# Optimization experiments

Measured on AMD Instinct MI355X. Metric: run time of the kernel, lower is better.

Reference implementation:

```python
import jax, jax.numpy as jnp
import numpy as np

NUM_EXPERTS = 8
TOP_K = 2
HIDDEN = 1024
INTER = 1408


def setup_inputs() -> dict:
    key = jax.random.key(0)
    k0, k1, k2, k3, k4 = jax.random.split(key, 5)
    B, S = 2, 2048
    d_scale = HIDDEN ** -0.5
    i_scale = INTER ** -0.5
    return {
        "hidden_states": jax.random.normal(k0, (B, S, HIDDEN), jnp.float32),
        # nn.Linear(hidden, num_experts, bias=False): weight (E, d)
        "gate_w": jax.random.normal(k1, (NUM_EXPERTS, HIDDEN), jnp.float32) * d_scale,
        # per-expert SwiGLU weights, nn.Linear convention (out, in)
        "gate_proj": jax.random.normal(k2, (NUM_EXPERTS, INTER, HIDDEN), jnp.float32) * d_scale,
        "up_proj": jax.random.normal(k3, (NUM_EXPERTS, INTER, HIDDEN), jnp.float32) * d_scale,
        "down_proj": jax.random.normal(k4, (NUM_EXPERTS, HIDDEN, INTER), jnp.float32) * i_scale,
    }


def reference(hidden_states, gate_w, gate_proj, up_proj, down_proj):
    B, S, D = hidden_states.shape
    x = hidden_states.reshape(-1, D)  # (T, d)
    T = x.shape[0]

    # gate linear -> router logits (T, E)
    router_logits = x @ gate_w.T

    # TopKRouter: softmax in fp32 over all experts, top-k, optional renorm
    probs = jax.nn.softmax(router_logits.astype(jnp.float32), axis=-1)
    routing_weights, selected_experts = jax.lax.top_k(probs, TOP_K)  # (T, k)
    routing_weights = routing_weights / routing_weights.sum(axis=-1, keepdims=True)  # norm_topk_prob
    routing_weights = routing_weights.astype(x.dtype)

    # combine weights per (token, expert): scatter top-k weights into dense (T, E)
    combine = jnp.zeros((T, NUM_EXPERTS), x.dtype).at[
        jnp.arange(T)[:, None], selected_experts
    ].add(routing_weights)

    # per-expert SwiGLU FFN, weighted combine (loop over small fixed expert set)
    out = jnp.zeros_like(x)
    for e in range(NUM_EXPERTS):
        h = jax.nn.silu(x @ gate_proj[e].T) * (x @ up_proj[e].T)  # (T, i)
        out = out + combine[:, e : e + 1] * (h @ down_proj[e].T)  # (T, d)

    return out.reshape(B, S, D), router_logits
```

## Files before the change

### kernel.cpp

```cpp
#include <hip/hip_runtime.h>
#include <hip/hip_bf16.h>
#include <stdint.h>

#define T_TOK 4096
#define DH 1024
#define DI 1408
#define NE 8
#define TOPK 2
#define PADROWS 9216

typedef short s16x8 __attribute__((ext_vector_type(8)));
typedef float f32x4 __attribute__((ext_vector_type(4)));

__device__ inline unsigned f2bf(float f) {
    __hip_bfloat16 h = __float2bfloat16(f);
    return (unsigned)*(unsigned short*)&h;
}
__device__ inline float bf2f(unsigned short u) {
    return __uint_as_float(((unsigned)u) << 16);
}

#define GLDS(src, dst) __builtin_amdgcn_global_load_lds( \
    (const __attribute__((address_space(1))) void*)(src), \
    (__attribute__((address_space(3))) void*)(dst), 16, 0, 0)

__global__ __launch_bounds__(256) void router_kernel(const float* __restrict__ x,
                              const float* __restrict__ gw,
                              float* __restrict__ logits_out,
                              int* __restrict__ tokE, float* __restrict__ tokW,
                              unsigned short* __restrict__ xb,
                              const float* __restrict__ gp, const float* __restrict__ up,
                              const float* __restrict__ dp,
                              unsigned short* __restrict__ gpb, unsigned short* __restrict__ upb,
                              unsigned short* __restrict__ dpb) {
    int wave = threadIdx.x >> 6;
    int lane = threadIdx.x & 63;
    int t = blockIdx.x * 4 + wave;
    const float4* xr = (const float4*)(x + (size_t)t * DH);

    float acc[NE];
#pragma unroll
    for (int e = 0; e < NE; ++e) acc[e] = 0.f;

#pragma unroll
    for (int i = 0; i < 4; ++i) {
        float4 xv = xr[lane + i * 64];
#pragma unroll
        for (int e = 0; e < NE; ++e) {
            float4 g = ((const float4*)(gw + (size_t)e * DH))[lane + i * 64];
            acc[e] += xv.x * g.x + xv.y * g.y + xv.z * g.z + xv.w * g.w;
        }
        uint2 o;
        o.x = f2bf(xv.x) | (f2bf(xv.y) << 16);
        o.y = f2bf(xv.z) | (f2bf(xv.w) << 16);
        *(uint2*)(xb + (size_t)t * DH + (lane + i * 64) * 4) = o;
    }
#pragma unroll
    for (int e = 0; e < NE; ++e) {
#pragma unroll
        for (int off = 32; off > 0; off >>= 1) acc[e] += __shfl_xor(acc[e], off, 64);
    }
    if (lane == 0) {
        float mx = acc[0];
#pragma unroll
        for (int e = 1; e < NE; ++e) mx = fmaxf(mx, acc[e]);
        float p[NE]; float s = 0.f;
#pragma unroll
        for (int e = 0; e < NE; ++e) { p[e] = expf(acc[e] - mx); s += p[e]; }
        float inv = 1.f / s;
#pragma unroll
        for (int e = 0; e < NE; ++e) p[e] *= inv;
        int i0 = 0, i1 = -1; float p0 = -1.f, p1 = -1.f;
#pragma unroll
        for (int e = 0; e < NE; ++e) {
            float v = p[e];
            if (v > p0) { p1 = p0; i1 = i0; p0 = v; i0 = e; }
            else if (v > p1) { p1 = v; i1 = e; }
        }
        float wsum = p0 + p1;
#pragma unroll
        for (int e = 0; e < NE; ++e) logits_out[(size_t)t * NE + e] = acc[e];
        tokE[2 * t]     = i0;  tokE[2 * t + 1] = i1;
        tokW[2 * t]     = p0 / wsum;  tokW[2 * t + 1] = p1 / wsum;
    }

    const int NW4 = NE * DI * DH / 4;
    const int NT = (T_TOK / 4) * 256;
    int gtid = blockIdx.x * 256 + threadIdx.x;
    for (int i = gtid; i < NW4; i += NT) {
        float4 v = ((const float4*)gp)[i];
        uint2 o;
        o.x = f2bf(v.x) | (f2bf(v.y) << 16);
        o.y = f2bf(v.z) | (f2bf(v.w) << 16);
        ((uint2*)gpb)[i] = o;
    }
    for (int i = gtid; i < NW4; i += NT) {
        float4 v = ((const float4*)up)[i];
        uint2 o;
        o.x = f2bf(v.x) | (f2bf(v.y) << 16);
        o.y = f2bf(v.z) | (f2bf(v.w) << 16);
        ((uint2*)upb)[i] = o;
    }
    for (int i = gtid; i < NW4; i += NT) {
        float4 v = ((const float4*)dp)[i];
        uint2 o;
        o.x = f2bf(v.x) | (f2bf(v.y) << 16);
        o.y = f2bf(v.z) | (f2bf(v.w) << 16);
        ((uint2*)dpb)[i] = o;
    }
}

__global__ __launch_bounds__(1024) void histscatter_kernel(const int* __restrict__ tokE,
        int* __restrict__ countsG, int* __restrict__ padOffG,
        int* __restrict__ assignTok, int* __restrict__ tokSlot) {
    __shared__ int wc[16][NE];
    __shared__ int padOff[NE + 1];
    __shared__ int cursor[NE];
    int tid = threadIdx.x, wave = tid >> 6, lane = tid & 63;

    int cnt[NE];
#pragma unroll
    for (int e = 0; e < NE; ++e) cnt[e] = 0;
    for (int i = tid; i < T_TOK * TOPK; i += 1024) {
        int v = tokE[i];
#pragma unroll
        for (int e = 0; e < NE; ++e)
            cnt[e] += (int)__popcll(__ballot(v == e));
    }
    if (lane == 0) {
#pragma unroll
        for (int e = 0; e < NE; ++e) wc[wave][e] = cnt[e];
    }
    __syncthreads();
    if (tid == 0) {
        int r = 0;
        for (int e = 0; e < NE; ++e) {
            int c = 0;
            for (int w = 0; w < 16; ++w) c += wc[w][e];
            countsG[e] = c;
            padOff[e] = r;
            padOffG[e] = r;
            cursor[e] = 0;
            r += ((c + 127) >> 7) << 7;
        }
        padOff[NE] = r;
        padOffG[NE] = r;
    }
    __syncthreads();

    unsigned long long lmask = (1ull << lane) - 1ull;
    for (int i = tid; i < T_TOK * TOPK; i += 1024) {
        int e = tokE[i];
#pragma unroll
        for (int ex = 0; ex < NE; ++ex) {
            unsigned long long m = __ballot(e == ex);
            if (e == ex) {
                int rank = (int)__popcll(m & lmask);
                int leader = __ffsll((long long)m) - 1;
                int b = 0;
                if (rank == 0) b = atomicAdd(&cursor[ex], (int)__popcll(m));
                b = __shfl(b, leader, 64);
                int slot = padOff[ex] + b + rank;
                assignTok[slot] = i >> 1;
                tokSlot[i] = slot;
            }
        }
    }
}

__global__ __launch_bounds__(512) void gemmA_kernel(
        const unsigned short* __restrict__ xb,
        const unsigned short* __restrict__ gpb, const unsigned short* __restrict__ upb,
        const int* __restrict__ padOff, const int* __restrict__ assignTok,
        unsigned short* __restrict__ h) {
    int bid = blockIdx.x;
    int nid = (bid & 7) * 99 + (bid >> 3);
    int colblk = nid / 72, rowblk = nid - colblk * 72;
    int pr0 = rowblk * 128;
    int n0 = colblk * 128;
    int e = -1;
#pragma unroll
    for (int i = 0; i < NE; ++i)
        if (pr0 >= padOff[i] && pr0 < padOff[i + 1]) e = i;
    if (e < 0) return;

    __shared__ unsigned short As[2][128 * 32];
    __shared__ unsigned short Bgs[2][128 * 32];
    __shared__ unsigned short Bus[2][128 * 32];

    int tid = threadIdx.x;
    int lane = tid & 63;
    int w = tid >> 6;
    int wm = (w >> 2) * 64;
    int wn = (w & 3) * 32;

    int srow = w * 16 + (lane >> 2);
    int aslot = (((lane & 3) ^ ((lane >> 3) & 3)) << 3);
    int tok = assignTok[pr0 + srow];
    const unsigned short* a0   = xb  + (size_t)tok * DH + aslot;
    const unsigned short* gsrc = gpb + ((size_t)e * DI + n0 + srow) * DH + aslot;
    const unsigned short* usrc = upb + ((size_t)e * DI + n0 + srow) * DH + aslot;
    int sdst = w * 512;

    int rq = (((lane >> 4) ^ ((lane >> 1) & 3)) << 3);

    f32x4 accG[4][2], accU[4][2];
#pragma unroll
    for (int i = 0; i < 4; ++i)
#pragma unroll
        for (int j = 0; j < 2; ++j) {
            accG[i][j] = (f32x4){0.f, 0.f, 0.f, 0.f};
            accU[i][j] = (f32x4){0.f, 0.f, 0.f, 0.f};
        }

#define STAGE_A(buf, k0) do { \
    GLDS(a0 + (k0),   &As[buf][sdst]); \
    GLDS(gsrc + (k0), &Bgs[buf][sdst]); \
    GLDS(usrc + (k0), &Bus[buf][sdst]); \
    } while (0)

#define KCOMP_A(cur, VMS) do { \
    asm volatile("s_waitcnt vmcnt(" VMS ")" ::: "memory"); \
    __builtin_amdgcn_s_barrier(); \
    __builtin_amdgcn_sched_barrier(0); \
    s16x8 af[4], bgf[2], bu2[2]; \
    _Pragma("unroll") \
    for (int i = 0; i < 4; ++i) \
        af[i] = *(const s16x8*)&As[cur][(wm + 16 * i + (lane & 15)) * 32 + rq]; \
    _Pragma("unroll") \
    for (int j = 0; j < 2; ++j) { \
        bgf[j] = *(const s16x8*)&Bgs[cur][(wn + 16 * j + (lane & 15)) * 32 + rq]; \
        bu2[j] = *(const s16x8*)&Bus[cur][(wn + 16 * j + (lane & 15)) * 32 + rq]; \
    } \
    _Pragma("unroll") \
    for (int i = 0; i < 4; ++i) \
        _Pragma("unroll") \
        for (int j = 0; j < 2; ++j) { \
            accG[i][j] = __builtin_amdgcn_mfma_f32_16x16x32_bf16(af[i], bgf[j], accG[i][j], 0, 0, 0); \
            accU[i][j] = __builtin_amdgcn_mfma_f32_16x16x32_bf16(af[i], bu2[j], accU[i][j], 0, 0, 0); \
        } \
    __builtin_amdgcn_sched_barrier(0); \
    __builtin_amdgcn_s_barrier(); \
    } while (0)

    STAGE_A(0, 0);
    for (int ks = 0; ks < 31; ++ks) {
        STAGE_A((ks + 1) & 1, (ks + 1) * 32);
        KCOMP_A(ks & 1, "3");
    }
    KCOMP_A(1, "0");
#undef STAGE_A
#undef KCOMP_A

#pragma unroll
    for (int i = 0; i < 4; ++i) {
        int rowb = pr0 + wm + 16 * i + ((lane >> 4) << 2);
#pragma unroll
        for (int j = 0; j < 2; ++j) {
            int col = n0 + wn + 16 * j + (lane & 15);
#pragma unroll
            for (int r = 0; r < 4; ++r) {
                float g = accG[i][j][r], u = accU[i][j][r];
                float val = (g / (1.f + __expf(-g))) * u;
                h[(size_t)(rowb + r) * DI + col] = (unsigned short)f2bf(val);
            }
        }
    }
}

__global__ __launch_bounds__(256) void gemmB_kernel(
        const unsigned short* __restrict__ h,
        const unsigned short* __restrict__ dpb,
        const int* __restrict__ padOff, const int* __restrict__ counts,
        unsigned short* __restrict__ outP) {
    int bid = blockIdx.x;
    int nid = (bid & 7) * 72 + (bid >> 3);
    int colblk = nid / 72, rowblk = nid - colblk * 72;
    int pr0 = rowblk * 128;
    int n0 = colblk * 128;
    int e = -1, base = 0;
#pragma unroll
    for (int i = 0; i < NE; ++i)
        if (pr0 >= padOff[i] && pr0 < padOff[i + 1]) { e = i; base = padOff[i]; }
    if (e < 0) return;
    int cnt = counts[e];

    __shared__ unsigned short As[2][128 * 32];
    __shared__ unsigned short Bs[2][128 * 32];

    int tid = threadIdx.x;
    int lane = tid & 63;
    int w = tid >> 6;
    int wm = (w >> 1) * 64;
    int wn = (w & 1) * 64;

    int srow = w * 32 + (lane >> 2);
    int aslot = (((lane & 3) ^ ((lane >> 3) & 3)) << 3);
    const unsigned short* a0   = h   + (size_t)(pr0 + srow) * DI + aslot;
    const unsigned short* a1   = h   + (size_t)(pr0 + srow + 16) * DI + aslot;
    const unsigned short* b0   = dpb + ((size_t)e * DH + n0 + srow) * DI + aslot;
    const unsigned short* b1   = dpb + ((size_t)e * DH + n0 + srow + 16) * DI + aslot;
    int sdst = w * 1024;

    int rq = (((lane >> 4) ^ ((lane >> 1) & 3)) << 3);

    f32x4 acc[4][4];
#pragma unroll
    for (int i = 0; i < 4; ++i)
#pragma unroll
        for (int j = 0; j < 4; ++j) acc[i][j] = (f32x4){0.f, 0.f, 0.f, 0.f};

#define STAGE_B(buf, k0) do { \
    GLDS(a0 + (k0), &As[buf][sdst]); \
    GLDS(a1 + (k0), &As[buf][sdst + 512]); \
    GLDS(b0 + (k0), &Bs[buf][sdst]); \
    GLDS(b1 + (k0), &Bs[buf][sdst + 512]); \
    } while (0)

#define KCOMP_B(cur, VMS) do { \
    asm volatile("s_waitcnt vmcnt(" VMS ")" ::: "memory"); \
    __builtin_amdgcn_s_barrier(); \
    __builtin_amdgcn_sched_barrier(0); \
    s16x8 af[4], bf[4]; \
    _Pragma("unroll") \
    for (int i = 0; i < 4; ++i) \
        af[i] = *(const s16x8*)&As[cur][(wm + 16 * i + (lane & 15)) * 32 + rq]; \
    _Pragma("unroll") \
    for (int j = 0; j < 4; ++j) \
        bf[j] = *(const s16x8*)&Bs[cur][(wn + 16 * j + (lane & 15)) * 32 + rq]; \
    _Pragma("unroll") \
    for (int i = 0; i < 4; ++i) \
        _Pragma("unroll") \
        for (int j = 0; j < 4; ++j) \
            acc[i][j] = __builtin_amdgcn_mfma_f32_16x16x32_bf16(af[i], bf[j], acc[i][j], 0, 0, 0); \
    __builtin_amdgcn_sched_barrier(0); \
    __builtin_amdgcn_s_barrier(); \
    } while (0)

    STAGE_B(0, 0);
    for (int ks = 0; ks < 43; ++ks) {
        STAGE_B((ks + 1) & 1, (ks + 1) * 32);
        KCOMP_B(ks & 1, "4");
    }
    KCOMP_B(1, "0");
#undef STAGE_B
#undef KCOMP_B

#pragma unroll
    for (int i = 0; i < 4; ++i) {
        int rowb = pr0 + wm + 16 * i + ((lane >> 4) << 2);
#pragma unroll
        for (int r = 0; r < 4; ++r) {
            int prow = rowb + r;
            if (prow - base < cnt) {
#pragma unroll
                for (int j = 0; j < 4; ++j) {
                    int col = n0 + wn + 16 * j + (lane & 15);
                    outP[(size_t)prow * DH + col] = (unsigned short)f2bf(acc[i][j][r]);
                }
            }
        }
    }
}

__global__ __launch_bounds__(256) void combine_kernel(const unsigned short* __restrict__ outP,
        const int* __restrict__ tokSlot, const float* __restrict__ tokW,
        float* __restrict__ out) {
    int t = blockIdx.x;
    int c = threadIdx.x * 4;
    int s0 = tokSlot[2 * t], s1 = tokSlot[2 * t + 1];
    float w0 = tokW[2 * t], w1 = tokW[2 * t + 1];
    ushort4 a = *(const ushort4*)(outP + (size_t)s0 * DH + c);
    ushort4 b = *(const ushort4*)(outP + (size_t)s1 * DH + c);
    float4 o;
    o.x = w0 * bf2f(a.x) + w1 * bf2f(b.x);
    o.y = w0 * bf2f(a.y) + w1 * bf2f(b.y);
    o.z = w0 * bf2f(a.z) + w1 * bf2f(b.z);
    o.w = w0 * bf2f(a.w) + w1 * bf2f(b.w);
    *(float4*)(out + (size_t)t * DH + c) = o;
}

extern "C" void kernel_launch(void* const* d_in, const int* in_sizes, int n_in,
                              void* d_out, int out_size, void* d_ws, size_t ws_size,
                              hipStream_t stream) {
    const float* x  = (const float*)d_in[0];
    const float* gw = (const float*)d_in[1];
    const float* gp = (const float*)d_in[2];
    const float* up = (const float*)d_in[3];
    const float* dp = (const float*)d_in[4];
    float* out = (float*)d_out;
    float* logits = out + (size_t)T_TOK * DH;

    char* ws = (char*)d_ws;
    int*   counts    = (int*)(ws + 0);
    int*   padOff    = (int*)(ws + 128);
    int*   tokE      = (int*)(ws + 4096);
    float* tokW      = (float*)(ws + 36864);
    int*   tokSlot   = (int*)(ws + 69632);
    int*   assignTok = (int*)(ws + 102400);
    unsigned short* xb   = (unsigned short*)(ws + 147456);
    unsigned short* gpb  = (unsigned short*)(ws + 8536064);
    unsigned short* upb  = (unsigned short*)(ws + 31604736);
    unsigned short* dpb  = (unsigned short*)(ws + 54673408);
    unsigned short* h    = (unsigned short*)(ws + 77742080);
    unsigned short* outP = (unsigned short*)(ws + 8536064);

    hipMemsetAsync(ws + 102400, 0, PADROWS * 4, stream);

    router_kernel<<<T_TOK / 4, 256, 0, stream>>>(x, gw, logits, tokE, tokW, xb,
                                                 gp, up, dp, gpb, upb, dpb);
    histscatter_kernel<<<1, 1024, 0, stream>>>(tokE, counts, padOff, assignTok, tokSlot);

    gemmA_kernel<<<dim3((DI / 128) * (PADROWS / 128)), 512, 0, stream>>>(xb, gpb, upb, padOff, assignTok, h);
    gemmB_kernel<<<dim3((DH / 128) * (PADROWS / 128)), 256, 0, stream>>>(h, dpb, padOff, counts, outP);
    combine_kernel<<<T_TOK, 256, 0, stream>>>(outP, tokSlot, tokW, out);
}
```

Before: 192.0 us.

## Split weight conversion into a wide kernel and move GEMM barriers before MFMAs

Fp32-to-bf16 conversion of the three expert weight tensors moves out of the router kernel into a separate kernel that handles 8 elements per thread with 16-byte stores, and it runs with a fixed 2048-block grid. In both GEMM inner loops, the trailing barrier after the MFMAs is replaced by an LDS-wait plus barrier placed right after the fragment reads. The next stage's global-to-LDS loads can then overlap the MFMA work instead of waiting for it. This adds one extra kernel launch. Moving the barrier relies on the double-buffer ordering staying race-free.

```diff
diff --git a/kernel.cpp b/kernel.cpp
--- a/kernel.cpp
+++ b/kernel.cpp
@@ -24,15 +24,34 @@
     (const __attribute__((address_space(1))) void*)(src), \
     (__attribute__((address_space(3))) void*)(dst), 16, 0, 0)
 
+__global__ __launch_bounds__(256) void cvt3_kernel(const float* __restrict__ s0,
+        const float* __restrict__ s1, const float* __restrict__ s2,
+        uint4* __restrict__ t0, uint4* __restrict__ t1, uint4* __restrict__ t2, int n8) {
+    int i = blockIdx.x * blockDim.x + threadIdx.x;
+    int stride = gridDim.x * blockDim.x;
+    const float4* f0 = (const float4*)s0;
+    const float4* f1 = (const float4*)s1;
+    const float4* f2 = (const float4*)s2;
+    for (; i < n8; i += stride) {
+        float4 a0 = f0[2 * i], b0 = f0[2 * i + 1];
+        float4 a1 = f1[2 * i], b1 = f1[2 * i + 1];
+        float4 a2 = f2[2 * i], b2 = f2[2 * i + 1];
+        uint4 o0, o1, o2;
+        o0.x = f2bf(a0.x) | (f2bf(a0.y) << 16); o0.y = f2bf(a0.z) | (f2bf(a0.w) << 16);
+        o0.z = f2bf(b0.x) | (f2bf(b0.y) << 16); o0.w = f2bf(b0.z) | (f2bf(b0.w) << 16);
+        o1.x = f2bf(a1.x) | (f2bf(a1.y) << 16); o1.y = f2bf(a1.z) | (f2bf(a1.w) << 16);
+        o1.z = f2bf(b1.x) | (f2bf(b1.y) << 16); o1.w = f2bf(b1.z) | (f2bf(b1.w) << 16);
+        o2.x = f2bf(a2.x) | (f2bf(a2.y) << 16); o2.y = f2bf(a2.z) | (f2bf(a2.w) << 16);
+        o2.z = f2bf(b2.x) | (f2bf(b2.y) << 16); o2.w = f2bf(b2.z) | (f2bf(b2.w) << 16);
+        t0[i] = o0; t1[i] = o1; t2[i] = o2;
+    }
+}
+
 __global__ __launch_bounds__(256) void router_kernel(const float* __restrict__ x,
                               const float* __restrict__ gw,
                               float* __restrict__ logits_out,
                               int* __restrict__ tokE, float* __restrict__ tokW,
-                              unsigned short* __restrict__ xb,
-                              const float* __restrict__ gp, const float* __restrict__ up,
-                              const float* __restrict__ dp,
-                              unsigned short* __restrict__ gpb, unsigned short* __restrict__ upb,
-                              unsigned short* __restrict__ dpb) {
+                              unsigned short* __restrict__ xb) {
     int wave = threadIdx.x >> 6;
     int lane = threadIdx.x & 63;
     int t = blockIdx.x * 4 + wave;
@@ -82,31 +101,6 @@
         for (int e = 0; e < NE; ++e) logits_out[(size_t)t * NE + e] = acc[e];
         tokE[2 * t]     = i0;  tokE[2 * t + 1] = i1;
         tokW[2 * t]     = p0 / wsum;  tokW[2 * t + 1] = p1 / wsum;
-    }
-
-    const int NW4 = NE * DI * DH / 4;
-    const int NT = (T_TOK / 4) * 256;
-    int gtid = blockIdx.x * 256 + threadIdx.x;
-    for (int i = gtid; i < NW4; i += NT) {
-        float4 v = ((const float4*)gp)[i];
-        uint2 o;
-        o.x = f2bf(v.x) | (f2bf(v.y) << 16);
-        o.y = f2bf(v.z) | (f2bf(v.w) << 16);
-        ((uint2*)gpb)[i] = o;
-    }
-    for (int i = gtid; i < NW4; i += NT) {
-        float4 v = ((const float4*)up)[i];
-        uint2 o;
-        o.x = f2bf(v.x) | (f2bf(v.y) << 16);
-        o.y = f2bf(v.z) | (f2bf(v.w) << 16);
-        ((uint2*)upb)[i] = o;
-    }
-    for (int i = gtid; i < NW4; i += NT) {
-        float4 v = ((const float4*)dp)[i];
-        uint2 o;
-        o.x = f2bf(v.x) | (f2bf(v.y) << 16);
-        o.y = f2bf(v.z) | (f2bf(v.w) << 16);
-        ((uint2*)dpb)[i] = o;
     }
 }
 
@@ -232,6 +226,10 @@
         bgf[j] = *(const s16x8*)&Bgs[cur][(wn + 16 * j + (lane & 15)) * 32 + rq]; \
         bu2[j] = *(const s16x8*)&Bus[cur][(wn + 16 * j + (lane & 15)) * 32 + rq]; \
     } \
+    asm volatile("s_waitcnt lgkmcnt(0)" ::: "memory"); \
+    __builtin_amdgcn_sched_barrier(0); \
+    __builtin_amdgcn_s_barrier(); \
+    __builtin_amdgcn_sched_barrier(0); \
     _Pragma("unroll") \
     for (int i = 0; i < 4; ++i) \
         _Pragma("unroll") \
@@ -239,8 +237,6 @@
             accG[i][j] = __builtin_amdgcn_mfma_f32_16x16x32_bf16(af[i], bgf[j], accG[i][j], 0, 0, 0); \
             accU[i][j] = __builtin_amdgcn_mfma_f32_16x16x32_bf16(af[i], bu2[j], accU[i][j], 0, 0, 0); \
         } \
-    __builtin_amdgcn_sched_barrier(0); \
-    __builtin_amdgcn_s_barrier(); \
     } while (0)
 
     STAGE_A(0, 0);
@@ -328,13 +324,15 @@
     _Pragma("unroll") \
     for (int j = 0; j < 4; ++j) \
         bf[j] = *(const s16x8*)&Bs[cur][(wn + 16 * j + (lane & 15)) * 32 + rq]; \
+    asm volatile("s_waitcnt lgkmcnt(0)" ::: "memory"); \
+    __builtin_amdgcn_sched_barrier(0); \
+    __builtin_amdgcn_s_barrier(); \
+    __builtin_amdgcn_sched_barrier(0); \
     _Pragma("unroll") \
     for (int i = 0; i < 4; ++i) \
         _Pragma("unroll") \
         for (int j = 0; j < 4; ++j) \
             acc[i][j] = __builtin_amdgcn_mfma_f32_16x16x32_bf16(af[i], bf[j], acc[i][j], 0, 0, 0); \
-    __builtin_amdgcn_sched_barrier(0); \
-    __builtin_amdgcn_s_barrier(); \
     } while (0)
 
     STAGE_B(0, 0);
@@ -407,8 +405,10 @@
 
     hipMemsetAsync(ws + 102400, 0, PADROWS * 4, stream);
 
-    router_kernel<<<T_TOK / 4, 256, 0, stream>>>(x, gw, logits, tokE, tokW, xb,
-                                                 gp, up, dp, gpb, upb, dpb);
+    const int NW8 = NE * DI * DH / 8;
+    cvt3_kernel<<<2048, 256, 0, stream>>>(gp, up, dp, (uint4*)gpb, (uint4*)upb, (uint4*)dpb, NW8);
+
+    router_kernel<<<T_TOK / 4, 256, 0, stream>>>(x, gw, logits, tokE, tokW, xb);
     histscatter_kernel<<<1, 1024, 0, stream>>>(tokE, counts, padOff, assignTok, tokSlot);
 
     gemmA_kernel<<<dim3((DI / 128) * (PADROWS / 128)), 512, 0, stream>>>(xb, gpb, upb, padOff, assignTok, h);
```

New measurement: 188.4 us. About the same (-1.8%).

## Split weight conversion into extra blocks and overlap down-proj cast with gemmA

Applied to the files above, without the earlier changes.

The fp32-to-bf16 weight conversion moves out of the router's token threads into dedicated extra blocks. The down_proj conversion now runs as 256 extra blocks appended to gemmA, so it overlaps the first GEMM instead of delaying the router. gemmA drops to 256 threads per block, each wave computing a 64x64 tile with more accumulators, and both GEMMs move the second barrier before the MFMA loop after waiting on LDS reads. This increases register pressure in gemmA and may reduce occupancy.

```diff
diff --git a/kernel.cpp b/kernel.cpp
--- a/kernel.cpp
+++ b/kernel.cpp
@@ -30,9 +30,27 @@
                               int* __restrict__ tokE, float* __restrict__ tokW,
                               unsigned short* __restrict__ xb,
                               const float* __restrict__ gp, const float* __restrict__ up,
-                              const float* __restrict__ dp,
-                              unsigned short* __restrict__ gpb, unsigned short* __restrict__ upb,
-                              unsigned short* __restrict__ dpb) {
+                              unsigned short* __restrict__ gpb, unsigned short* __restrict__ upb) {
+    if (blockIdx.x >= T_TOK / 4) {
+        const int NW4 = NE * DI * DH / 4;
+        const int stride = (T_TOK / 4) * 256;
+        int i0 = (blockIdx.x - T_TOK / 4) * 256 + threadIdx.x;
+        for (int i = i0; i < NW4; i += stride) {
+            float4 v = ((const float4*)gp)[i];
+            uint2 o;
+            o.x = f2bf(v.x) | (f2bf(v.y) << 16);
+            o.y = f2bf(v.z) | (f2bf(v.w) << 16);
+            ((uint2*)gpb)[i] = o;
+        }
+        for (int i = i0; i < NW4; i += stride) {
+            float4 v = ((const float4*)up)[i];
+            uint2 o;
+            o.x = f2bf(v.x) | (f2bf(v.y) << 16);
+            o.y = f2bf(v.z) | (f2bf(v.w) << 16);
+            ((uint2*)upb)[i] = o;
+        }
+        return;
+    }
     int wave = threadIdx.x >> 6;
     int lane = threadIdx.x & 63;
     int t = blockIdx.x * 4 + wave;
@@ -82,31 +100,6 @@
         for (int e = 0; e < NE; ++e) logits_out[(size_t)t * NE + e] = acc[e];
         tokE[2 * t]     = i0;  tokE[2 * t + 1] = i1;
         tokW[2 * t]     = p0 / wsum;  tokW[2 * t + 1] = p1 / wsum;
-    }
-
-    const int NW4 = NE * DI * DH / 4;
-    const int NT = (T_TOK / 4) * 256;
-    int gtid = blockIdx.x * 256 + threadIdx.x;
-    for (int i = gtid; i < NW4; i += NT) {
-        float4 v = ((const float4*)gp)[i];
-        uint2 o;
-        o.x = f2bf(v.x) | (f2bf(v.y) << 16);
-        o.y = f2bf(v.z) | (f2bf(v.w) << 16);
-        ((uint2*)gpb)[i] = o;
-    }
-    for (int i = gtid; i < NW4; i += NT) {
-        float4 v = ((const float4*)up)[i];
-        uint2 o;
-        o.x = f2bf(v.x) | (f2bf(v.y) << 16);
-        o.y = f2bf(v.z) | (f2bf(v.w) << 16);
-        ((uint2*)upb)[i] = o;
-    }
-    for (int i = gtid; i < NW4; i += NT) {
-        float4 v = ((const float4*)dp)[i];
-        uint2 o;
-        o.x = f2bf(v.x) | (f2bf(v.y) << 16);
-        o.y = f2bf(v.z) | (f2bf(v.w) << 16);
-        ((uint2*)dpb)[i] = o;
     }
 }
 
@@ -168,12 +161,25 @@
     }
 }
 
-__global__ __launch_bounds__(512) void gemmA_kernel(
+__global__ __launch_bounds__(256) void gemmA_kernel(
         const unsigned short* __restrict__ xb,
         const unsigned short* __restrict__ gpb, const unsigned short* __restrict__ upb,
         const int* __restrict__ padOff, const int* __restrict__ assignTok,
-        unsigned short* __restrict__ h) {
+        unsigned short* __restrict__ h,
+        const float* __restrict__ dp, unsigned short* __restrict__ dpb) {
     int bid = blockIdx.x;
+    if (bid >= 792) {
+        const int NW4 = NE * DI * DH / 4;
+        const int stride = 256 * 256;
+        for (int i = (bid - 792) * 256 + threadIdx.x; i < NW4; i += stride) {
+            float4 v = ((const float4*)dp)[i];
+            uint2 o;
+            o.x = f2bf(v.x) | (f2bf(v.y) << 16);
+            o.y = f2bf(v.z) | (f2bf(v.w) << 16);
+            ((uint2*)dpb)[i] = o;
+        }
+        return;
+    }
     int nid = (bid & 7) * 99 + (bid >> 3);
     int colblk = nid / 72, rowblk = nid - colblk * 72;
     int pr0 = rowblk * 128;
@@ -191,62 +197,72 @@
     int tid = threadIdx.x;
     int lane = tid & 63;
     int w = tid >> 6;
-    int wm = (w >> 2) * 64;
-    int wn = (w & 3) * 32;
+    int wm = (w >> 1) * 64;
+    int wn = (w & 1) * 64;
 
     int srow = w * 16 + (lane >> 2);
     int aslot = (((lane & 3) ^ ((lane >> 3) & 3)) << 3);
-    int tok = assignTok[pr0 + srow];
-    const unsigned short* a0   = xb  + (size_t)tok * DH + aslot;
-    const unsigned short* gsrc = gpb + ((size_t)e * DI + n0 + srow) * DH + aslot;
-    const unsigned short* usrc = upb + ((size_t)e * DI + n0 + srow) * DH + aslot;
-    int sdst = w * 512;
+    int tok0 = assignTok[pr0 + srow];
+    int tok1 = assignTok[pr0 + 64 + srow];
+    const unsigned short* a0 = xb + (size_t)tok0 * DH + aslot;
+    const unsigned short* a1 = xb + (size_t)tok1 * DH + aslot;
+    const unsigned short* g0 = gpb + ((size_t)e * DI + n0 + srow) * DH + aslot;
+    const unsigned short* g1 = gpb + ((size_t)e * DI + n0 + 64 + srow) * DH + aslot;
+    const unsigned short* u0 = upb + ((size_t)e * DI + n0 + srow) * DH + aslot;
+    const unsigned short* u1 = upb + ((size_t)e * DI + n0 + 64 + srow) * DH + aslot;
+    int sd0 = w * 512;
+    int sd1 = 2048 + w * 512;
 
     int rq = (((lane >> 4) ^ ((lane >> 1) & 3)) << 3);
 
-    f32x4 accG[4][2], accU[4][2];
+    f32x4 accG[4][4], accU[4][4];
 #pragma unroll
     for (int i = 0; i < 4; ++i)
 #pragma unroll
-        for (int j = 0; j < 2; ++j) {
+        for (int j = 0; j < 4; ++j) {
             accG[i][j] = (f32x4){0.f, 0.f, 0.f, 0.f};
             accU[i][j] = (f32x4){0.f, 0.f, 0.f, 0.f};
         }
 
 #define STAGE_A(buf, k0) do { \
-    GLDS(a0 + (k0),   &As[buf][sdst]); \
-    GLDS(gsrc + (k0), &Bgs[buf][sdst]); \
-    GLDS(usrc + (k0), &Bus[buf][sdst]); \
+    GLDS(a0 + (k0), &As[buf][sd0]); \
+    GLDS(a1 + (k0), &As[buf][sd1]); \
+    GLDS(g0 + (k0), &Bgs[buf][sd0]); \
+    GLDS(g1 + (k0), &Bgs[buf][sd1]); \
+    GLDS(u0 + (k0), &Bus[buf][sd0]); \
+    GLDS(u1 + (k0), &Bus[buf][sd1]); \
     } while (0)
 
 #define KCOMP_A(cur, VMS) do { \
     asm volatile("s_waitcnt vmcnt(" VMS ")" ::: "memory"); \
     __builtin_amdgcn_s_barrier(); \
     __builtin_amdgcn_sched_barrier(0); \
-    s16x8 af[4], bgf[2], bu2[2]; \
+    s16x8 af[4], bgf[4], bu2[4]; \
     _Pragma("unroll") \
     for (int i = 0; i < 4; ++i) \
         af[i] = *(const s16x8*)&As[cur][(wm + 16 * i + (lane & 15)) * 32 + rq]; \
     _Pragma("unroll") \
-    for (int j = 0; j < 2; ++j) { \
+    for (int j = 0; j < 4; ++j) { \
         bgf[j] = *(const s16x8*)&Bgs[cur][(wn + 16 * j + (lane & 15)) * 32 + rq]; \
         bu2[j] = *(const s16x8*)&Bus[cur][(wn + 16 * j + (lane & 15)) * 32 + rq]; \
     } \
+    asm volatile("s_waitcnt lgkmcnt(0)" ::: "memory"); \
+    __builtin_amdgcn_sched_barrier(0); \
+    __builtin_amdgcn_s_barrier(); \
+    __builtin_amdgcn_sched_barrier(0); \
     _Pragma("unroll") \
     for (int i = 0; i < 4; ++i) \
         _Pragma("unroll") \
-        for (int j = 0; j < 2; ++j) { \
+        for (int j = 0; j < 4; ++j) { \
             accG[i][j] = __builtin_amdgcn_mfma_f32_16x16x32_bf16(af[i], bgf[j], accG[i][j], 0, 0, 0); \
             accU[i][j] = __builtin_amdgcn_mfma_f32_16x16x32_bf16(af[i], bu2[j], accU[i][j], 0, 0, 0); \
         } \
-    __builtin_amdgcn_sched_barrier(0); \
-    __builtin_amdgcn_s_barrier(); \
     } while (0)
 
     STAGE_A(0, 0);
     for (int ks = 0; ks < 31; ++ks) {
         STAGE_A((ks + 1) & 1, (ks + 1) * 32);
-        KCOMP_A(ks & 1, "3");
+        KCOMP_A(ks & 1, "6");
     }
     KCOMP_A(1, "0");
 #undef STAGE_A
@@ -256,7 +272,7 @@
     for (int i = 0; i < 4; ++i) {
         int rowb = pr0 + wm + 16 * i + ((lane >> 4) << 2);
 #pragma unroll
-        for (int j = 0; j < 2; ++j) {
+        for (int j = 0; j < 4; ++j) {
             int col = n0 + wn + 16 * j + (lane & 15);
 #pragma unroll
             for (int r = 0; r < 4; ++r) {
@@ -328,13 +344,15 @@
     _Pragma("unroll") \
     for (int j = 0; j < 4; ++j) \
         bf[j] = *(const s16x8*)&Bs[cur][(wn + 16 * j + (lane & 15)) * 32 + rq]; \
+    asm volatile("s_waitcnt lgkmcnt(0)" ::: "memory"); \
+    __builtin_amdgcn_sched_barrier(0); \
+    __builtin_amdgcn_s_barrier(); \
+    __builtin_amdgcn_sched_barrier(0); \
     _Pragma("unroll") \
     for (int i = 0; i < 4; ++i) \
         _Pragma("unroll") \
         for (int j = 0; j < 4; ++j) \
             acc[i][j] = __builtin_amdgcn_mfma_f32_16x16x32_bf16(af[i], bf[j], acc[i][j], 0, 0, 0); \
-    __builtin_amdgcn_sched_barrier(0); \
-    __builtin_amdgcn_s_barrier(); \
     } while (0)
 
     STAGE_B(0, 0);
@@ -407,11 +425,11 @@
 
     hipMemsetAsync(ws + 102400, 0, PADROWS * 4, stream);
 
-    router_kernel<<<T_TOK / 4, 256, 0, stream>>>(x, gw, logits, tokE, tokW, xb,
-                                                 gp, up, dp, gpb, upb, dpb);
+    router_kernel<<<2 * (T_TOK / 4), 256, 0, stream>>>(x, gw, logits, tokE, tokW, xb,
+                                                       gp, up, gpb, upb);
     histscatter_kernel<<<1, 1024, 0, stream>>>(tokE, counts, padOff, assignTok, tokSlot);
 
-    gemmA_kernel<<<dim3((DI / 128) * (PADROWS / 128)), 512, 0, stream>>>(xb, gpb, upb, padOff, assignTok, h);
-    gemmB_kernel<<<dim3((DH / 128) * (PADROWS / 128)), 256, 0, stream>>>(h, dpb, padOff, counts, outP);
+    gemmA_kernel<<<792 + 256, 256, 0, stream>>>(xb, gpb, upb, padOff, assignTok, h, dp, dpb);
+    gemmB_kernel<<<(DH / 128) * (PADROWS / 128), 256, 0, stream>>>(h, dpb, padOff, counts, outP);
     combine_kernel<<<T_TOK, 256, 0, stream>>>(outP, tokSlot, tokW, out);
 }
```

New measurement: 204.4 us. 1.06x slower.
